# Kernel optimization log

Hardware: AMD Instinct MI355X
Metric: run time of the kernel (lower is better)

## Reference

```python
import jax, jax.numpy as jnp
import numpy as np

EMBED_DIM = 1024
N_HEADS = 16
HEAD_DIM = EMBED_DIM // N_HEADS
B, T = 1, 4096

def setup_inputs() -> dict:
    key = jax.random.key(0)
    k1, k2, k3 = jax.random.split(key, 3)
    x = jax.random.normal(k1, (B, T, EMBED_DIM), dtype=jnp.float32)
    # match nn.Linear init scale roughly (not required for correctness testing)
    w_qkv = jax.random.normal(k2, (EMBED_DIM, 3 * EMBED_DIM), dtype=jnp.float32) * (EMBED_DIM ** -0.5)
    w_out = jax.random.normal(k3, (EMBED_DIM, EMBED_DIM), dtype=jnp.float32) * (EMBED_DIM ** -0.5)
    return {"x": x, "w_qkv": w_qkv, "w_out": w_out}

def reference(x, w_qkv, w_out):
    b, t, c = x.shape
    qkv = x @ w_qkv                                  # [B,T,3C]
    q, k, v = jnp.split(qkv, 3, axis=-1)
    # [B,T,C] -> [B,H,T,D]
    def heads(a):
        return a.reshape(b, t, N_HEADS, HEAD_DIM).transpose(0, 2, 1, 3)
    q, k, v = heads(q), heads(k), heads(v)
    scale = 1.0 / jnp.sqrt(jnp.asarray(HEAD_DIM, dtype=x.dtype))
    att = jnp.einsum('bhqd,bhkd->bhqk', q, k) * scale  # [B,H,T,T] (full matrix, as in source)
    att = jax.nn.softmax(att, axis=-1)
    y = jnp.einsum('bhqk,bhkd->bhqd', att, v)          # [B,H,T,D]
    y = y.transpose(0, 2, 1, 3).reshape(b, t, c)
    return y @ w_out
```

## Files before the change

### kernel.cpp

```cpp
#include <hip/hip_runtime.h>
#include <hip/hip_bf16.h>

#define T_SEQ 4096
#define C_DIM 1024
#define NH    16
#define HD    64
#define C3    3072

typedef __attribute__((ext_vector_type(8))) short short8;
typedef __attribute__((ext_vector_type(4))) short short4v;
typedef __attribute__((ext_vector_type(4))) float f32x4;
typedef __attribute__((ext_vector_type(16))) float f32x16;

__device__ __forceinline__ short f2bf(float f) {
  union { float f; unsigned u; } v; v.f = f;
  unsigned r = v.u + 0x7FFFu + ((v.u >> 16) & 1u);
  return (short)(r >> 16);
}

__device__ __forceinline__ unsigned cvt_pk_bf16(float lo, float hi) {
  unsigned r;
  asm volatile("v_cvt_pk_bf16_f32 %0, %1, %2" : "=v"(r) : "v"(lo), "v"(hi));
  return r;
}

__device__ __forceinline__ float exp2_fast(float x) {
  return __builtin_amdgcn_exp2f(x);
}

__device__ __forceinline__ float max_half64(float v) {
  return fmaxf(v, __shfl_xor(v, 32, 64));
}
__device__ __forceinline__ float sum_half64(float v) {
  return v + __shfl_xor(v, 32, 64);
}

__device__ __forceinline__ float m3(float a, float b, float c) {
  return fmaxf(fmaxf(a, b), c);
}

__device__ __forceinline__ void gld_lds16(const void* g, void* l) {
  __builtin_amdgcn_global_load_lds(
      (const __attribute__((address_space(1))) unsigned int*)g,
      (__attribute__((address_space(3))) unsigned int*)l, 16, 0, 0);
}

__global__ __launch_bounds__(256) void conv_bf16_kernel(const float* __restrict__ in,
                                                        short* __restrict__ out) {
  const size_t i = ((size_t)blockIdx.x * 256 + threadIdx.x) * 8;
  float4 v0 = *(const float4*)(in + i);
  float4 v1 = *(const float4*)(in + i + 4);
  short8 o;
  o[0] = f2bf(v0.x); o[1] = f2bf(v0.y); o[2] = f2bf(v0.z); o[3] = f2bf(v0.w);
  o[4] = f2bf(v1.x); o[5] = f2bf(v1.y); o[6] = f2bf(v1.z); o[7] = f2bf(v1.w);
  *(short8*)(out + i) = o;
}

__global__ void trans_conv_kernel(const float* __restrict__ in, short* __restrict__ out,
                                  int K, int N) {
  __shared__ float t[32][33];
  const int n0 = blockIdx.x * 32, k0 = blockIdx.y * 32;
  const int tx = threadIdx.x, ty = threadIdx.y;
  for (int i = ty; i < 32; i += 8) t[i][tx] = in[(size_t)(k0 + i) * N + n0 + tx];
  __syncthreads();
  for (int i = ty; i < 32; i += 8) out[(size_t)(n0 + i) * K + k0 + tx] = f2bf(t[tx][i]);
}

__device__ __forceinline__ void store_out(short* C, size_t idx, float v) { C[idx] = f2bf(v); }
__device__ __forceinline__ void store_out(float* C, size_t idx, float v) { C[idx] = v; }

template <typename OutT>
__global__ __launch_bounds__(256) void gemm_bt_kernel(const short* __restrict__ A,
                                                      const short* __restrict__ BT,
                                                      OutT* __restrict__ C,
                                                      int M, int N, int K) {
  __shared__ __align__(16) short As[128 * 32];
  __shared__ __align__(16) short Bs[128 * 32];
  const int tid = threadIdx.x;
  const int wid = tid >> 6;
  const int lane = tid & 63;
  const int l15 = lane & 15;
  const int l4 = lane >> 4;
  const int wr = wid >> 1;
  const int wc = wid & 1;
  const int bm = blockIdx.y * 128;
  const int bn = blockIdx.x * 128;

  f32x4 acc[4][4];
#pragma unroll
  for (int m = 0; m < 4; ++m)
#pragma unroll
    for (int n = 0; n < 4; ++n) acc[m][n] = (f32x4){0.f, 0.f, 0.f, 0.f};

  const int ebase = wid * 1024;
  const int e0 = ebase + lane * 8;
  const int r0 = e0 >> 5, c0 = e0 & 31;
  const int r1 = r0 + 16;

  for (int k0 = 0; k0 < K; k0 += 32) {
    __syncthreads();
    gld_lds16(A + (size_t)(bm + r0) * K + k0 + c0, As + ebase);
    gld_lds16(A + (size_t)(bm + r1) * K + k0 + c0, As + ebase + 512);
    gld_lds16(BT + (size_t)(bn + r0) * K + k0 + c0, Bs + ebase);
    gld_lds16(BT + (size_t)(bn + r1) * K + k0 + c0, Bs + ebase + 512);
    __syncthreads();

    short8 a[4], b[4];
#pragma unroll
    for (int m = 0; m < 4; ++m)
      a[m] = *(const short8*)&As[(wr * 64 + m * 16 + l15) * 32 + l4 * 8];
#pragma unroll
    for (int n = 0; n < 4; ++n)
      b[n] = *(const short8*)&Bs[(wc * 64 + n * 16 + l15) * 32 + l4 * 8];
#pragma unroll
    for (int m = 0; m < 4; ++m)
#pragma unroll
      for (int n = 0; n < 4; ++n)
        acc[m][n] = __builtin_amdgcn_mfma_f32_16x16x32_bf16(a[m], b[n], acc[m][n], 0, 0, 0);
  }

#pragma unroll
  for (int m = 0; m < 4; ++m) {
    const int row0 = bm + wr * 64 + m * 16 + l4 * 4;
#pragma unroll
    for (int n = 0; n < 4; ++n) {
      const int col = bn + wc * 64 + n * 16 + l15;
#pragma unroll
      for (int r = 0; r < 4; ++r)
        store_out(C, (size_t)(row0 + r) * N + col, acc[m][n][r]);
    }
  }
}

__global__ __launch_bounds__(256) void repack_v_kernel(const short* __restrict__ qkv,
                                                       short* __restrict__ vT) {
  const int h = blockIdx.x >> 6;
  const int t0 = (blockIdx.x & 63) << 6;
  __shared__ __align__(16) short tile[64][72];
  const int t = threadIdx.x;
  const int r = t >> 3, c = (t & 7) << 3;
#pragma unroll
  for (int i = 0; i < 2; ++i) {
    const int rr = r + i * 32;
    *(short8*)&tile[rr][c] =
        *(const short8*)&qkv[(size_t)(t0 + rr) * C3 + 2048 + h * 64 + c];
  }
  __syncthreads();
  const int d = t >> 3, tt = (t & 7) << 3;
#pragma unroll
  for (int i = 0; i < 2; ++i) {
    const int dd = d + i * 32;
    short8 v;
#pragma unroll
    for (int j = 0; j < 8; ++j) v[j] = tile[tt + j][dd];
    *(short8*)&vT[(size_t)(h * 64 + dd) * T_SEQ + t0 + tt] = v;
  }
}

__global__ __launch_bounds__(512, 4) void attn_kernel(const short* __restrict__ qkv,
                                                      const short* __restrict__ vT,
                                                      short* __restrict__ y) {
  const int bid = blockIdx.x;
  const int xcd = bid & 7, slot = bid >> 3;
  const int h = xcd * 2 + (slot >> 5);
  const int q0 = (slot & 31) * 128;

  const int tid = threadIdx.x;
  const int w = tid >> 6, lane = tid & 63, l31 = lane & 31, l1 = lane >> 5;
  const int g = w >> 2, wg = w & 3;
  const int kvbase = g * (T_SEQ / 2);

  __shared__ __align__(16) short Ks[2][2][4096];
  __shared__ __align__(16) short Vs[2][2][4096];

  short8 qf[4];
  {
    const short* qp = qkv + (size_t)(q0 + wg * 32 + l31) * C3 + h * 64 + l1 * 8;
#pragma unroll
    for (int ks = 0; ks < 4; ++ks) qf[ks] = *(const short8*)(qp + ks * 16);
  }

  f32x16 oa0, oa1;
#pragma unroll
  for (int r = 0; r < 16; ++r) { oa0[r] = 0.f; oa1[r] = 0.f; }
  float m_r = -INFINITY, l_r = 0.f;
  const float SCL = 0.125f * 1.44269504f;
  const float TH = 8.0f / SCL;

  const int lr0 = wg * 8 + (lane >> 3);
  const int csw = ((lane & 7) << 3) ^ ((lane >> 3) << 3);
  const short* kpt = qkv + 1024 + h * 64 + csw + (size_t)(kvbase + lr0) * C3;
  const short* vpt = vT + (size_t)(h * 64 + lr0) * T_SEQ + csw + kvbase;
  const int rswz = (l31 & 7) << 3;

  auto stage = [&](int buf) {
#pragma unroll
    for (int i = 0; i < 2; ++i) {
      gld_lds16(kpt + (size_t)i * 32 * C3, &Ks[g][buf][i * 2048 + wg * 512]);
      gld_lds16(vpt + (size_t)i * 32 * T_SEQ, &Vs[g][buf][i * 2048 + wg * 512]);
    }
  };

  stage(0);
  kpt += (size_t)64 * C3;
  vpt += 64;

  const int NT = T_SEQ / 2 / 64;
  for (int t = 0; t < NT; ++t) {
    const int cur = t & 1;
    __builtin_amdgcn_s_barrier();
    if (t + 1 < NT) {
      stage(cur ^ 1);
      kpt += (size_t)64 * C3;
      vpt += 64;
      asm volatile("s_waitcnt vmcnt(4)" ::: "memory");
    } else {
      asm volatile("s_waitcnt vmcnt(0)" ::: "memory");
    }
    __builtin_amdgcn_s_barrier();

    const short* Kb = &Ks[g][cur][0];
    const short* Vb = &Vs[g][cur][0];

    f32x16 s0, s1;
#pragma unroll
    for (int r = 0; r < 16; ++r) { s0[r] = 0.f; s1[r] = 0.f; }
    __builtin_amdgcn_s_setprio(1);
#pragma unroll
    for (int ks = 0; ks < 4; ++ks) {
      const int c = (ks * 16 + l1 * 8) ^ rswz;
      short8 k0 = *(const short8*)&Kb[l31 * 64 + c];
      short8 k1 = *(const short8*)&Kb[(32 + l31) * 64 + c];
      s0 = __builtin_amdgcn_mfma_f32_32x32x16_bf16(k0, qf[ks], s0, 0, 0, 0);
      s1 = __builtin_amdgcn_mfma_f32_32x32x16_bf16(k1, qf[ks], s1, 0, 0, 0);
    }
    __builtin_amdgcn_s_setprio(0);

    float tm;
    {
      float v0 = m3(s0[0], s0[1], s0[2]);
      float v1 = m3(s0[3], s0[4], s0[5]);
      float v2 = m3(s0[6], s0[7], s0[8]);
      float v3 = m3(s0[9], s0[10], s0[11]);
      float v4 = m3(s0[12], s0[13], s0[14]);
      float v5 = fmaxf(s0[15], s1[0]);
      float v6 = m3(s1[1], s1[2], s1[3]);
      float v7 = m3(s1[4], s1[5], s1[6]);
      float v8 = m3(s1[7], s1[8], s1[9]);
      float v9 = m3(s1[10], s1[11], s1[12]);
      float v10 = m3(s1[13], s1[14], s1[15]);
      float w0 = m3(v0, v1, v2);
      float w1 = m3(v3, v4, v5);
      float w2 = m3(v6, v7, v8);
      float w3 = fmaxf(v9, v10);
      tm = fmaxf(m3(w0, w1, w2), w3);
    }
    tm = max_half64(tm);

    if (__any(tm > m_r + TH)) {
      const float mn = fmaxf(m_r, tm);
      const float al = exp2_fast((m_r - mn) * SCL);
      m_r = mn;
      l_r *= al;
#pragma unroll
      for (int r = 0; r < 16; ++r) { oa0[r] *= al; oa1[r] *= al; }
    }
    const float msc = m_r * SCL;
#pragma unroll
    for (int r = 0; r < 16; ++r) s0[r] = exp2_fast(fmaf(s0[r], SCL, -msc));
#pragma unroll
    for (int r = 0; r < 16; ++r) s1[r] = exp2_fast(fmaf(s1[r], SCL, -msc));

    float ps;
    {
      float u8[8];
#pragma unroll
      for (int r = 0; r < 8; ++r)
        u8[r] = (s0[r] + s0[r + 8]) + (s1[r] + s1[r + 8]);
#pragma unroll
      for (int r = 0; r < 4; ++r) u8[r] += u8[r + 4];
      ps = (u8[0] + u8[2]) + (u8[1] + u8[3]);
    }
    ps = sum_half64(ps);
    l_r += ps;

    unsigned pw[4][4];
#pragma unroll
    for (int half = 0; half < 2; ++half) {
      const f32x16& sv = half ? s1 : s0;
#pragma unroll
      for (int kk = 0; kk < 2; ++kk) {
        const int ks = half * 2 + kk;
        unsigned x0 = cvt_pk_bf16(sv[kk * 8 + 0], sv[kk * 8 + 1]);
        unsigned y0 = cvt_pk_bf16(sv[kk * 8 + 4], sv[kk * 8 + 5]);
        asm volatile("s_nop 0\n\tv_permlane32_swap_b32 %0, %1" : "+v"(x0), "+v"(y0));
        unsigned x1 = cvt_pk_bf16(sv[kk * 8 + 2], sv[kk * 8 + 3]);
        unsigned y1 = cvt_pk_bf16(sv[kk * 8 + 6], sv[kk * 8 + 7]);
        asm volatile("s_nop 0\n\tv_permlane32_swap_b32 %0, %1" : "+v"(x1), "+v"(y1));
        pw[ks][0] = x0; pw[ks][1] = x1; pw[ks][2] = y0; pw[ks][3] = y1;
      }
    }

    __builtin_amdgcn_s_setprio(1);
#pragma unroll
    for (int ks = 0; ks < 4; ++ks) {
      union { unsigned u[4]; short8 s8; } uu;
      uu.u[0] = pw[ks][0]; uu.u[1] = pw[ks][1]; uu.u[2] = pw[ks][2]; uu.u[3] = pw[ks][3];
      const int c = (ks * 16 + l1 * 8) ^ rswz;
      short8 v0 = *(const short8*)&Vb[l31 * 64 + c];
      short8 v1 = *(const short8*)&Vb[(32 + l31) * 64 + c];
      oa0 = __builtin_amdgcn_mfma_f32_32x32x16_bf16(v0, uu.s8, oa0, 0, 0, 0);
      oa1 = __builtin_amdgcn_mfma_f32_32x32x16_bf16(v1, uu.s8, oa1, 0, 0, 0);
    }
    __builtin_amdgcn_s_setprio(0);
  }

  __syncthreads();
  float* Oex = (float*)&Vs[0][0][0];
  float* mex = (float*)&Ks[0][0][0];
  const int xslot = wg * 64 + lane;
  if (g == 1) {
#pragma unroll
    for (int r = 0; r < 16; ++r) {
      Oex[r * 256 + xslot] = oa0[r];
      Oex[(16 + r) * 256 + xslot] = oa1[r];
    }
    mex[xslot] = m_r;
    mex[256 + xslot] = l_r;
  }
  __syncthreads();
  if (g == 0) {
    const float m_b = mex[xslot], l_b = mex[256 + xslot];
    const float mm = fmaxf(m_r, m_b);
    const float a = exp2_fast((m_r - mm) * SCL);
    const float b = exp2_fast((m_b - mm) * SCL);
    const float rl = 1.0f / (l_r * a + l_b * b);
    const float ra = a * rl, rb = b * rl;
    const size_t yb = (size_t)(q0 + wg * 32 + l31) * C_DIM + h * 64;
#pragma unroll
    for (int g4 = 0; g4 < 4; ++g4) {
      short4v o0, o1;
#pragma unroll
      for (int j = 0; j < 4; ++j) {
        o0[j] = f2bf(oa0[g4 * 4 + j] * ra + Oex[(g4 * 4 + j) * 256 + xslot] * rb);
        o1[j] = f2bf(oa1[g4 * 4 + j] * ra + Oex[(16 + g4 * 4 + j) * 256 + xslot] * rb);
      }
      *(short4v*)&y[yb + g4 * 8 + l1 * 4] = o0;
      *(short4v*)&y[yb + 32 + g4 * 8 + l1 * 4] = o1;
    }
  }
}

extern "C" void kernel_launch(void* const* d_in, const int* in_sizes, int n_in,
                              void* d_out, int out_size, void* d_ws, size_t ws_size,
                              hipStream_t stream) {
  const float* x = (const float*)d_in[0];
  const float* w_qkv = (const float*)d_in[1];
  const float* w_out = (const float*)d_in[2];
  float* out = (float*)d_out;

  char* ws = (char*)d_ws;
  short* xb = (short*)ws;            ws += (size_t)T_SEQ * C_DIM * 2;
  short* wqT = (short*)ws;           ws += (size_t)C3 * C_DIM * 2;
  short* woT = (short*)ws;           ws += (size_t)C_DIM * C_DIM * 2;
  short* qkv = (short*)ws;           ws += (size_t)T_SEQ * C3 * 2;
  short* vT = (short*)ws;            ws += (size_t)NH * T_SEQ * HD * 2;
  short* y = (short*)ws;             ws += (size_t)T_SEQ * C_DIM * 2;

  conv_bf16_kernel<<<(T_SEQ * C_DIM) / (256 * 8), 256, 0, stream>>>(x, xb);
  trans_conv_kernel<<<dim3(C3 / 32, C_DIM / 32), dim3(32, 8), 0, stream>>>(w_qkv, wqT, C_DIM, C3);
  trans_conv_kernel<<<dim3(C_DIM / 32, C_DIM / 32), dim3(32, 8), 0, stream>>>(w_out, woT, C_DIM, C_DIM);

  gemm_bt_kernel<short><<<dim3(C3 / 128, T_SEQ / 128), 256, 0, stream>>>(xb, wqT, qkv,
                                                                         T_SEQ, C3, C_DIM);
  repack_v_kernel<<<NH * (T_SEQ / 64), 256, 0, stream>>>(qkv, vT);

  attn_kernel<<<512, 512, 0, stream>>>(qkv, vT, y);

  gemm_bt_kernel<float><<<dim3(C_DIM / 128, T_SEQ / 128), 256, 0, stream>>>(y, woT, out,
                                                                            T_SEQ, C_DIM, C_DIM);
}
```

Baseline: 180.0 us.

## Split attention KV halves across blocks and merge partials in separate kernel

Before, each 512-thread block ran both KV halves in two wave groups and merged them in LDS. Now each half gets its own 256-thread block (1024 blocks), which writes fp32 partial outputs plus max/sum stats to global memory. A new merge kernel then combines the halves and writes bf16 y. This gives more, smaller blocks and halves the LDS per block, which may improve occupancy and scheduling, but it adds about 33MB of fp32 partial traffic and one extra kernel launch.

Result: slower. 189.1 us (+5.1%).

```diff
diff --git a/kernel.cpp b/kernel.cpp
--- a/kernel.cpp
+++ b/kernel.cpp
@@ -157,25 +157,26 @@
   }
 }
 
-__global__ __launch_bounds__(512, 4) void attn_kernel(const short* __restrict__ qkv,
+__global__ __launch_bounds__(256, 4) void attn_kernel(const short* __restrict__ qkv,
                                                       const short* __restrict__ vT,
-                                                      short* __restrict__ y) {
+                                                      float* __restrict__ Opart,
+                                                      float* __restrict__ MLpart) {
   const int bid = blockIdx.x;
-  const int xcd = bid & 7, slot = bid >> 3;
-  const int h = xcd * 2 + (slot >> 5);
-  const int q0 = (slot & 31) * 128;
+  const int xcd = bid & 7, rest = bid >> 3;
+  const int s = xcd * 4 + (rest >> 5);
+  const int h = s >> 1, half = s & 1;
+  const int q0 = (rest & 31) * 128;
+  const int kvbase = half * (T_SEQ / 2);
 
   const int tid = threadIdx.x;
   const int w = tid >> 6, lane = tid & 63, l31 = lane & 31, l1 = lane >> 5;
-  const int g = w >> 2, wg = w & 3;
-  const int kvbase = g * (T_SEQ / 2);
-
-  __shared__ __align__(16) short Ks[2][2][4096];
-  __shared__ __align__(16) short Vs[2][2][4096];
+
+  __shared__ __align__(16) short Ks[2][4096];
+  __shared__ __align__(16) short Vs[2][4096];
 
   short8 qf[4];
   {
-    const short* qp = qkv + (size_t)(q0 + wg * 32 + l31) * C3 + h * 64 + l1 * 8;
+    const short* qp = qkv + (size_t)(q0 + w * 32 + l31) * C3 + h * 64 + l1 * 8;
 #pragma unroll
     for (int ks = 0; ks < 4; ++ks) qf[ks] = *(const short8*)(qp + ks * 16);
   }
@@ -187,7 +188,7 @@
   const float SCL = 0.125f * 1.44269504f;
   const float TH = 8.0f / SCL;
 
-  const int lr0 = wg * 8 + (lane >> 3);
+  const int lr0 = w * 8 + (lane >> 3);
   const int csw = ((lane & 7) << 3) ^ ((lane >> 3) << 3);
   const short* kpt = qkv + 1024 + h * 64 + csw + (size_t)(kvbase + lr0) * C3;
   const short* vpt = vT + (size_t)(h * 64 + lr0) * T_SEQ + csw + kvbase;
@@ -196,8 +197,8 @@
   auto stage = [&](int buf) {
 #pragma unroll
     for (int i = 0; i < 2; ++i) {
-      gld_lds16(kpt + (size_t)i * 32 * C3, &Ks[g][buf][i * 2048 + wg * 512]);
-      gld_lds16(vpt + (size_t)i * 32 * T_SEQ, &Vs[g][buf][i * 2048 + wg * 512]);
+      gld_lds16(kpt + (size_t)i * 32 * C3, &Ks[buf][i * 2048 + w * 512]);
+      gld_lds16(vpt + (size_t)i * 32 * T_SEQ, &Vs[buf][i * 2048 + w * 512]);
     }
   };
 
@@ -219,8 +220,8 @@
     }
     __builtin_amdgcn_s_barrier();
 
-    const short* Kb = &Ks[g][cur][0];
-    const short* Vb = &Vs[g][cur][0];
+    const short* Kb = &Ks[cur][0];
+    const short* Vb = &Vs[cur][0];
 
     f32x16 s0, s1;
 #pragma unroll
@@ -286,11 +287,11 @@
 
     unsigned pw[4][4];
 #pragma unroll
-    for (int half = 0; half < 2; ++half) {
-      const f32x16& sv = half ? s1 : s0;
+    for (int half2 = 0; half2 < 2; ++half2) {
+      const f32x16& sv = half2 ? s1 : s0;
 #pragma unroll
       for (int kk = 0; kk < 2; ++kk) {
-        const int ks = half * 2 + kk;
+        const int ks = half2 * 2 + kk;
         unsigned x0 = cvt_pk_bf16(sv[kk * 8 + 0], sv[kk * 8 + 1]);
         unsigned y0 = cvt_pk_bf16(sv[kk * 8 + 4], sv[kk * 8 + 5]);
         asm volatile("s_nop 0\n\tv_permlane32_swap_b32 %0, %1" : "+v"(x0), "+v"(y0));
@@ -315,39 +316,51 @@
     __builtin_amdgcn_s_setprio(0);
   }
 
-  __syncthreads();
-  float* Oex = (float*)&Vs[0][0][0];
-  float* mex = (float*)&Ks[0][0][0];
-  const int xslot = wg * 64 + lane;
-  if (g == 1) {
-#pragma unroll
-    for (int r = 0; r < 16; ++r) {
-      Oex[r * 256 + xslot] = oa0[r];
-      Oex[(16 + r) * 256 + xslot] = oa1[r];
-    }
-    mex[xslot] = m_r;
-    mex[256 + xslot] = l_r;
-  }
-  __syncthreads();
-  if (g == 0) {
-    const float m_b = mex[xslot], l_b = mex[256 + xslot];
-    const float mm = fmaxf(m_r, m_b);
-    const float a = exp2_fast((m_r - mm) * SCL);
-    const float b = exp2_fast((m_b - mm) * SCL);
-    const float rl = 1.0f / (l_r * a + l_b * b);
-    const float ra = a * rl, rb = b * rl;
-    const size_t yb = (size_t)(q0 + wg * 32 + l31) * C_DIM + h * 64;
-#pragma unroll
-    for (int g4 = 0; g4 < 4; ++g4) {
-      short4v o0, o1;
-#pragma unroll
-      for (int j = 0; j < 4; ++j) {
-        o0[j] = f2bf(oa0[g4 * 4 + j] * ra + Oex[(g4 * 4 + j) * 256 + xslot] * rb);
-        o1[j] = f2bf(oa1[g4 * 4 + j] * ra + Oex[(16 + g4 * 4 + j) * 256 + xslot] * rb);
-      }
-      *(short4v*)&y[yb + g4 * 8 + l1 * 4] = o0;
-      *(short4v*)&y[yb + 32 + g4 * 8 + l1 * 4] = o1;
-    }
+  const size_t row = (size_t)h * T_SEQ + q0 + w * 32 + l31;
+  const size_t obase = ((size_t)half * NH * T_SEQ + row) * 64;
+#pragma unroll
+  for (int g4 = 0; g4 < 4; ++g4) {
+    float4 f0 = {oa0[g4 * 4 + 0], oa0[g4 * 4 + 1], oa0[g4 * 4 + 2], oa0[g4 * 4 + 3]};
+    float4 f1 = {oa1[g4 * 4 + 0], oa1[g4 * 4 + 1], oa1[g4 * 4 + 2], oa1[g4 * 4 + 3]};
+    *(float4*)&Opart[obase + g4 * 8 + l1 * 4] = f0;
+    *(float4*)&Opart[obase + 32 + g4 * 8 + l1 * 4] = f1;
+  }
+  if (l1 == 0) {
+    *(float2*)&MLpart[((size_t)half * NH * T_SEQ + row) * 2] = {m_r, l_r};
+  }
+}
+
+__global__ __launch_bounds__(256) void merge_kernel(const float* __restrict__ Opart,
+                                                    const float* __restrict__ MLpart,
+                                                    short* __restrict__ y) {
+  const int tid = threadIdx.x;
+  const size_t row = (size_t)blockIdx.x * 64 + (tid >> 2);
+  const int dch = (tid & 3) * 16;
+  const int h = (int)(row >> 12), q = (int)(row & 4095);
+  const float SCL = 0.125f * 1.44269504f;
+
+  const float m0 = MLpart[row * 2], l0 = MLpart[row * 2 + 1];
+  const float m1 = MLpart[((size_t)NH * T_SEQ + row) * 2];
+  const float l1v = MLpart[((size_t)NH * T_SEQ + row) * 2 + 1];
+  const float mm = fmaxf(m0, m1);
+  const float a = exp2_fast((m0 - mm) * SCL);
+  const float b = exp2_fast((m1 - mm) * SCL);
+  const float rl = 1.0f / (l0 * a + l1v * b);
+  const float ra = a * rl, rb = b * rl;
+
+  const size_t o0 = row * 64 + dch;
+  const size_t o1 = (size_t)NH * T_SEQ * 64 + row * 64 + dch;
+  short* yp = y + (size_t)q * C_DIM + h * 64 + dch;
+#pragma unroll
+  for (int jj = 0; jj < 4; ++jj) {
+    float4 p0 = *(const float4*)&Opart[o0 + jj * 4];
+    float4 p1 = *(const float4*)&Opart[o1 + jj * 4];
+    short4v o;
+    o[0] = f2bf(p0.x * ra + p1.x * rb);
+    o[1] = f2bf(p0.y * ra + p1.y * rb);
+    o[2] = f2bf(p0.z * ra + p1.z * rb);
+    o[3] = f2bf(p0.w * ra + p1.w * rb);
+    *(short4v*)&yp[jj * 4] = o;
   }
 }
 
@@ -366,6 +379,8 @@
   short* qkv = (short*)ws;           ws += (size_t)T_SEQ * C3 * 2;
   short* vT = (short*)ws;            ws += (size_t)NH * T_SEQ * HD * 2;
   short* y = (short*)ws;             ws += (size_t)T_SEQ * C_DIM * 2;
+  float* Opart = (float*)ws;         ws += (size_t)2 * NH * T_SEQ * 64 * 4;
+  float* MLpart = (float*)ws;        ws += (size_t)2 * NH * T_SEQ * 2 * 4;
 
   conv_bf16_kernel<<<(T_SEQ * C_DIM) / (256 * 8), 256, 0, stream>>>(x, xb);
   trans_conv_kernel<<<dim3(C3 / 32, C_DIM / 32), dim3(32, 8), 0, stream>>>(w_qkv, wqT, C_DIM, C3);
@@ -375,7 +390,9 @@
                                                                          T_SEQ, C3, C_DIM);
   repack_v_kernel<<<NH * (T_SEQ / 64), 256, 0, stream>>>(qkv, vT);
 
-  attn_kernel<<<512, 512, 0, stream>>>(qkv, vT, y);
+  attn_kernel<<<1024, 256, 0, stream>>>(qkv, vT, Opart, MLpart);
+
+  merge_kernel<<<1024, 256, 0, stream>>>(Opart, MLpart, y);
 
   gemm_bt_kernel<float><<<dim3(C_DIM / 128, T_SEQ / 128), 256, 0, stream>>>(y, woT, out,
                                                                             T_SEQ, C_DIM, C_DIM);
```
